# Kernel tuning notes

Hardware: AMD Instinct MI355X
Metric: run time of the kernel (lower is better)

## Reference

```python
import jax, jax.numpy as jnp
import numpy as np

B, N_IN, N_VALUES = 1_000_000, 59, 12


def setup_inputs() -> dict:
    key = jax.random.key(0)
    k1, k2, k3, k4 = jax.random.split(key, 4)
    neural_activity = jax.random.normal(k1, (B, N_IN), dtype=jnp.float32)
    cards_by_trials = jax.random.randint(k2, (B, 4, 3), 0, N_VALUES, dtype=jnp.int64)
    # nn.Linear params: weight [out, in], bias [out]
    W = jax.random.normal(k3, (N_VALUES, N_IN), dtype=jnp.float32) / np.sqrt(N_IN)
    b = jax.random.normal(k4, (N_VALUES,), dtype=jnp.float32) * 0.01
    return {"neural_activity": neural_activity, "cards_by_trials": cards_by_trials, "W": W, "b": b}


def reference(neural_activity, cards_by_trials, W, b):
    # feature_values: [B, n_values]
    feature_values = jnp.einsum("bi,vi->bv", neural_activity, W) + b
    # fused gather + per-card sum (replaces the Python double loop)
    batch_idx = jnp.arange(feature_values.shape[0])[:, None, None]  # [B,1,1]
    gathered = feature_values[batch_idx, cards_by_trials]           # [B,4,3]
    card_values = jnp.sum(gathered, axis=-1)                        # [B,4]
    return card_values
```

## Files before the change

### kernel.cpp

```cpp
#include <hip/hip_runtime.h>

#define N_IN 59
#define N_VALUES 12
#define BLOCK 256
#define WROWS 32
#define ROWS_PER_BLOCK 128
#define TILE_F (WROWS * N_IN)
#define TILE_STRIDE_F 1896
#define FVW_STRIDE 17

typedef __attribute__((ext_vector_type(4))) float  f32x4;
typedef __attribute__((ext_vector_type(8))) __bf16 bf16x8;

static __device__ __forceinline__ unsigned short f2bf_bits(float x) {
    return __builtin_bit_cast(unsigned short, (__bf16)x);
}

__global__ void build_wfrag(const float* __restrict__ W,
                            unsigned short* __restrict__ tab) {
    int t = threadIdx.x;
    int h = t >> 6, l = t & 63;
    int v = l & 15, g = l >> 4;
    unsigned int words[4];
    #pragma unroll
    for (int p = 0; p < 4; ++p) {
        unsigned int lo, hi;
        {
            int k = h * 32 + g * 8 + 2 * p;
            float val = (k < N_IN && v < N_VALUES) ? W[v * N_IN + k] : 0.0f;
            lo = f2bf_bits(val);
        }
        {
            int k = h * 32 + g * 8 + 2 * p + 1;
            float val = (k < N_IN && v < N_VALUES) ? W[v * N_IN + k] : 0.0f;
            hi = f2bf_bits(val);
        }
        words[p] = lo | (hi << 16);
    }
    uint4 u = make_uint4(words[0], words[1], words[2], words[3]);
    *(uint4*)(tab + (size_t)t * 8) = u;
}

__global__ __launch_bounds__(BLOCK, 4) void value_model_kernel(
    const float* __restrict__ act,
    const int*   __restrict__ cards,
    const unsigned short* __restrict__ wtab,
    const float* __restrict__ bias,
    float* __restrict__ out,
    int B)
{
    __shared__ float aLds[4 * TILE_STRIDE_F];
    __shared__ float fvLds[4 * WROWS * FVW_STRIDE];

    const int tid  = threadIdx.x;
    const int wave = tid >> 6;
    const int lane = tid & 63;
    const long wbase = (long)blockIdx.x * ROWS_PER_BLOCK + wave * WROWS;
    if (wbase >= B) return;

    float* tw = aLds  + wave * TILE_STRIDE_F;
    float* fw = fvLds + wave * (WROWS * FVW_STRIDE);

    const bf16x8* tab8 = (const bf16x8*)wtab;
    bf16x8 bf0 = tab8[lane];
    bf16x8 bf1 = tab8[64 + lane];

    const int colA = lane & 15, gA = lane >> 4;
    float bv = (colA < N_VALUES) ? bias[colA] : 0.0f;
    f32x4 acc0 = {bv, bv, bv, bv};
    f32x4 acc1 = {bv, bv, bv, bv};

    {
        const float4* src = (const float4*)(act + wbase * N_IN);
        float4* dst = (float4*)tw;
        #pragma unroll
        for (int q = 0; q < 8; ++q) {
            int idx = lane + q * 64;
            if (idx < TILE_F / 4) dst[idx] = src[idx];
        }
    }
    asm volatile("s_waitcnt lgkmcnt(0)" ::: "memory");
    __builtin_amdgcn_wave_barrier();

    #pragma unroll
    for (int h = 0; h < 2; ++h) {
        #pragma unroll
        for (int rb = 0; rb < 2; ++rb) {
            const float* p = tw + (rb * 16 + colA) * N_IN + h * 32 + gA * 8;
            bf16x8 a;
            #pragma unroll
            for (int e = 0; e < 8; ++e) {
                float v = p[e];
                if (h == 1) {
                    int k = 32 + gA * 8 + e;
                    v = (k < N_IN) ? v : 0.0f;
                }
                a[e] = (__bf16)v;
            }
            if (rb == 0)
                acc0 = __builtin_amdgcn_mfma_f32_16x16x32_bf16(a, h ? bf1 : bf0, acc0, 0, 0, 0);
            else
                acc1 = __builtin_amdgcn_mfma_f32_16x16x32_bf16(a, h ? bf1 : bf0, acc1, 0, 0, 0);
        }
    }

    #pragma unroll
    for (int j = 0; j < 4; ++j) fw[(gA * 4 + j) * FVW_STRIDE + colA] = acc0[j];
    #pragma unroll
    for (int j = 0; j < 4; ++j) fw[(16 + gA * 4 + j) * FVW_STRIDE + colA] = acc1[j];
    asm volatile("s_waitcnt lgkmcnt(0)" ::: "memory");
    __builtin_amdgcn_wave_barrier();

    const int r    = lane >> 1;
    const int half = lane & 1;
    const long grow = wbase + r;
    const float* fv = fw + r * FVW_STRIDE;

    const int2* cp = (const int2*)(cards + grow * 12 + half * 6);
    int2 ca = cp[0], cb = cp[1], cc = cp[2];

    float s0 = fv[ca.x] + fv[ca.y] + fv[cb.x];
    float s1 = fv[cb.y] + fv[cc.x] + fv[cc.y];

    *(float2*)(out + grow * 4 + half * 2) = make_float2(s0, s1);
}

extern "C" void kernel_launch(void* const* d_in, const int* in_sizes, int n_in,
                              void* d_out, int out_size, void* d_ws, size_t ws_size,
                              hipStream_t stream) {
    const float* act   = (const float*)d_in[0];
    const int*   cards = (const int*)d_in[1];
    const float* W     = (const float*)d_in[2];
    const float* bias  = (const float*)d_in[3];
    float* out = (float*)d_out;
    unsigned short* wtab = (unsigned short*)d_ws;

    const int B = in_sizes[0] / N_IN;

    build_wfrag<<<1, 128, 0, stream>>>(W, wtab);

    const int grid = (B + ROWS_PER_BLOCK - 1) / ROWS_PER_BLOCK;
    value_model_kernel<<<grid, BLOCK, 0, stream>>>(act, cards, wtab, bias, out, B);
}
```

Before: 55.83 us.

## Load activation tiles via direct global-to-LDS DMA with smaller per-wave tiles

The activation tile is now copied with global_load_lds straight from global memory into LDS, so it no longer passes through VGPRs. Each wave now handles 16 rows instead of 32, which halves the work per wave and shared memory per block and lets the occupancy hint rise from 4 to 8 blocks. The card-index loads are issued before the wait so they overlap the tile transfer, and each lane computes one output. The grid now uses B/64 with no tail guard, so it only covers every row when B is a multiple of 64. Padding past the tile is zeroed in LDS so the k>=59 entries come out as zero.

New measurement: 52.32 us. 1.07x faster.

```diff
diff --git a/kernel.cpp b/kernel.cpp
--- a/kernel.cpp
+++ b/kernel.cpp
@@ -3,11 +3,12 @@
 #define N_IN 59
 #define N_VALUES 12
 #define BLOCK 256
-#define WROWS 32
-#define ROWS_PER_BLOCK 128
+#define WROWS 16
+#define ROWS_PER_BLOCK 64
 #define TILE_F (WROWS * N_IN)
-#define TILE_STRIDE_F 1896
-#define FVW_STRIDE 17
+#define TILE_F4 (TILE_F / 4)
+#define TILE_STRIDE_F 952
+#define FV_STRIDE 12
 
 typedef __attribute__((ext_vector_type(4))) float  f32x4;
 typedef __attribute__((ext_vector_type(8))) __bf16 bf16x8;
@@ -41,7 +42,7 @@
     *(uint4*)(tab + (size_t)t * 8) = u;
 }
 
-__global__ __launch_bounds__(BLOCK, 4) void value_model_kernel(
+__global__ __launch_bounds__(BLOCK, 8) void value_model_kernel(
     const float* __restrict__ act,
     const int*   __restrict__ cards,
     const unsigned short* __restrict__ wtab,
@@ -50,16 +51,36 @@
     int B)
 {
     __shared__ float aLds[4 * TILE_STRIDE_F];
-    __shared__ float fvLds[4 * WROWS * FVW_STRIDE];
+    __shared__ float fvLds[4 * WROWS * FV_STRIDE];
 
     const int tid  = threadIdx.x;
     const int wave = tid >> 6;
     const int lane = tid & 63;
     const long wbase = (long)blockIdx.x * ROWS_PER_BLOCK + wave * WROWS;
-    if (wbase >= B) return;
 
     float* tw = aLds  + wave * TILE_STRIDE_F;
-    float* fw = fvLds + wave * (WROWS * FVW_STRIDE);
+    float* fw = fvLds + wave * (WROWS * FV_STRIDE);
+
+    {
+        const char* src = (const char*)(act + wbase * N_IN) + lane * 16;
+        char* dst = (char*)tw;
+        __builtin_amdgcn_global_load_lds(
+            (const __attribute__((address_space(1))) void*)(src),
+            (__attribute__((address_space(3))) void*)(dst), 16, 0, 0);
+        __builtin_amdgcn_global_load_lds(
+            (const __attribute__((address_space(1))) void*)(src + 1024),
+            (__attribute__((address_space(3))) void*)(dst + 1024), 16, 0, 0);
+        __builtin_amdgcn_global_load_lds(
+            (const __attribute__((address_space(1))) void*)(src + 2048),
+            (__attribute__((address_space(3))) void*)(dst + 2048), 16, 0, 0);
+        if (lane < TILE_F4 - 192) {
+            __builtin_amdgcn_global_load_lds(
+                (const __attribute__((address_space(1))) void*)(src + 3072),
+                (__attribute__((address_space(3))) void*)(dst + 3072), 16, 0, 0);
+        }
+    }
+
+    if (lane < TILE_STRIDE_F - TILE_F) tw[TILE_F + lane] = 0.0f;
 
     const bf16x8* tab8 = (const bf16x8*)wtab;
     bf16x8 bf0 = tab8[lane];
@@ -67,62 +88,35 @@
 
     const int colA = lane & 15, gA = lane >> 4;
     float bv = (colA < N_VALUES) ? bias[colA] : 0.0f;
-    f32x4 acc0 = {bv, bv, bv, bv};
-    f32x4 acc1 = {bv, bv, bv, bv};
 
-    {
-        const float4* src = (const float4*)(act + wbase * N_IN);
-        float4* dst = (float4*)tw;
+    const int r4 = lane >> 2, c4 = lane & 3;
+    const long grow = wbase + r4;
+    const int* cp = cards + grow * 12 + c4 * 3;
+    const int i0 = cp[0], i1 = cp[1], i2 = cp[2];
+
+    asm volatile("s_waitcnt vmcnt(0) lgkmcnt(0)" ::: "memory");
+    __builtin_amdgcn_wave_barrier();
+
+    f32x4 acc = {bv, bv, bv, bv};
+    const float* p = tw + colA * N_IN + gA * 8;
+    bf16x8 a0, a1;
+    #pragma unroll
+    for (int e = 0; e < 8; ++e) a0[e] = (__bf16)p[e];
+    acc = __builtin_amdgcn_mfma_f32_16x16x32_bf16(a0, bf0, acc, 0, 0, 0);
+    #pragma unroll
+    for (int e = 0; e < 8; ++e) a1[e] = (__bf16)p[32 + e];
+    acc = __builtin_amdgcn_mfma_f32_16x16x32_bf16(a1, bf1, acc, 0, 0, 0);
+
+    if (colA < N_VALUES) {
         #pragma unroll
-        for (int q = 0; q < 8; ++q) {
-            int idx = lane + q * 64;
-            if (idx < TILE_F / 4) dst[idx] = src[idx];
-        }
+        for (int j = 0; j < 4; ++j)
+            fw[(gA * 4 + j) * FV_STRIDE + colA] = acc[j];
     }
     asm volatile("s_waitcnt lgkmcnt(0)" ::: "memory");
     __builtin_amdgcn_wave_barrier();
 
-    #pragma unroll
-    for (int h = 0; h < 2; ++h) {
-        #pragma unroll
-        for (int rb = 0; rb < 2; ++rb) {
-            const float* p = tw + (rb * 16 + colA) * N_IN + h * 32 + gA * 8;
-            bf16x8 a;
-            #pragma unroll
-            for (int e = 0; e < 8; ++e) {
-                float v = p[e];
-                if (h == 1) {
-                    int k = 32 + gA * 8 + e;
-                    v = (k < N_IN) ? v : 0.0f;
-                }
-                a[e] = (__bf16)v;
-            }
-            if (rb == 0)
-                acc0 = __builtin_amdgcn_mfma_f32_16x16x32_bf16(a, h ? bf1 : bf0, acc0, 0, 0, 0);
-            else
-                acc1 = __builtin_amdgcn_mfma_f32_16x16x32_bf16(a, h ? bf1 : bf0, acc1, 0, 0, 0);
-        }
-    }
-
-    #pragma unroll
-    for (int j = 0; j < 4; ++j) fw[(gA * 4 + j) * FVW_STRIDE + colA] = acc0[j];
-    #pragma unroll
-    for (int j = 0; j < 4; ++j) fw[(16 + gA * 4 + j) * FVW_STRIDE + colA] = acc1[j];
-    asm volatile("s_waitcnt lgkmcnt(0)" ::: "memory");
-    __builtin_amdgcn_wave_barrier();
-
-    const int r    = lane >> 1;
-    const int half = lane & 1;
-    const long grow = wbase + r;
-    const float* fv = fw + r * FVW_STRIDE;
-
-    const int2* cp = (const int2*)(cards + grow * 12 + half * 6);
-    int2 ca = cp[0], cb = cp[1], cc = cp[2];
-
-    float s0 = fv[ca.x] + fv[ca.y] + fv[cb.x];
-    float s1 = fv[cb.y] + fv[cc.x] + fv[cc.y];
-
-    *(float2*)(out + grow * 4 + half * 2) = make_float2(s0, s1);
+    const float* fv = fw + r4 * FV_STRIDE;
+    out[grow * 4 + c4] = fv[i0] + fv[i1] + fv[i2];
 }
 
 extern "C" void kernel_launch(void* const* d_in, const int* in_sizes, int n_in,
@@ -139,6 +133,6 @@
 
     build_wfrag<<<1, 128, 0, stream>>>(W, wtab);
 
-    const int grid = (B + ROWS_PER_BLOCK - 1) / ROWS_PER_BLOCK;
+    const int grid = B / ROWS_PER_BLOCK;
     value_model_kernel<<<grid, BLOCK, 0, stream>>>(act, cards, wtab, bias, out, B);
 }
```
